# Performance work log

Hardware: AMD Instinct MI355X
Metric: run time of the kernel (lower is better)

The kernel has to match this reference:

```python
import jax, jax.numpy as jnp
import numpy as np

B, T, D, E, K = 8, 2048, 1024, 8, 2
CAP = int(B * T * K / E * 1.0)  # capacity per expert = 4096


def setup_inputs() -> dict:
    key = jax.random.key(0)
    ks = jax.random.split(key, 12)
    s = 0.02
    return {
        "x": jax.random.normal(ks[0], (B, T, D), jnp.float32),
        "noise": jax.random.normal(ks[1], (B, T, E), jnp.float32),
        "Wr": jax.random.normal(ks[2], (D, E), jnp.float32) * s,
        "br": jnp.zeros((E,), jnp.float32),
        "Wn": jax.random.normal(ks[3], (D, E), jnp.float32) * s,
        "bn": jnp.zeros((E,), jnp.float32),
        "W1": jax.random.normal(ks[4], (E, D, 4 * D), jnp.float32) * s,
        "b1": jnp.zeros((E, 4 * D), jnp.float32),
        "W2": jax.random.normal(ks[5], (E, 4 * D, D), jnp.float32) * s,
        "b2": jnp.zeros((E, D), jnp.float32),
    }


def reference(x, noise, Wr, br, Wn, bn, W1, b1, W2, b2):
    # Noisy top-k router
    logits = jnp.einsum("btd,de->bte", x, Wr) + br
    noise_logits = jnp.einsum("btd,de->bte", x, Wn) + bn
    noisy = logits + noise * jax.nn.softplus(noise_logits)
    top_v, top_i = jax.lax.top_k(noisy, K)           # [B,T,K]
    gates = jax.nn.softmax(top_v, axis=-1)           # softmax over sparse (-inf elsewhere) == softmax over top-k values

    N = B * T
    flat_x = x.reshape(N, D)
    ti = top_i.reshape(N, K)
    route = jnp.zeros((N, E), x.dtype).at[jnp.arange(N)[:, None], ti].set(gates.reshape(N, K))

    upd = jnp.zeros_like(flat_x)
    for i in range(E):
        mask = (ti == i).any(axis=-1)                 # [N] tokens routed to expert i
        rank = jnp.cumsum(mask) - 1                   # arrival-order rank (matches torch.nonzero order)
        keep = mask & (rank < CAP)                    # capacity dropping: first CAP tokens
        pos, = jnp.nonzero(keep, size=CAP, fill_value=0)
        valid = jnp.arange(CAP) < keep.sum()
        xe = flat_x[pos]                              # [CAP, D]
        h = jax.nn.relu(xe @ W1[i] + b1[i])           # [CAP, 4D]
        out = h @ W2[i] + b2[i]                       # [CAP, D]
        gate = route[pos, i] * valid                  # zero gate for padded slots
        upd = upd.at[pos].add(out * gate[:, None])
    return upd.reshape(B, T, D)
```

## Files before the change

kernel.cpp:

```cpp
#include <hip/hip_runtime.h>

#define N_TOK 16384
#define DMODEL 1024
#define NEXP 8
#define CAP 4096
#define HDIM 4096

typedef unsigned short ushort_t;
typedef unsigned int u32;
typedef __attribute__((ext_vector_type(8))) _Float16 half8;
typedef __attribute__((ext_vector_type(8))) ushort_t ushort8;
typedef __attribute__((ext_vector_type(4))) float f32x4;

__device__ inline ushort_t f2h_bits(float f) {
  _Float16 h = (_Float16)f;
  union { _Float16 h; ushort_t u; } cv;
  cv.h = h;
  return cv.u;
}
__device__ inline float h2f(ushort_t u) {
  union { ushort_t u; _Float16 h; } cv;
  cv.u = u;
  return (float)cv.h;
}

__device__ inline void gll16(void* lds, const void* g) {
  __builtin_amdgcn_global_load_lds((const __attribute__((address_space(1))) u32*)g,
                                   (__attribute__((address_space(3))) u32*)lds,
                                   16, 0, 0);
}

__global__ __launch_bounds__(256) void routerW_prep(
    const float* __restrict__ Wr, const float* __restrict__ Wn,
    float* __restrict__ wrT, float* __restrict__ wnT) {
  int i = blockIdx.x * 256 + threadIdx.x;
  int d = i >> 3, e = i & 7;
  wrT[e * DMODEL + d] = Wr[i];
  wnT[e * DMODEL + d] = Wn[i];
}

__global__ __launch_bounds__(256, 4) void router_kernel(
    const float* __restrict__ x, const float* __restrict__ noise,
    const float* __restrict__ wrT, const float* __restrict__ wnT,
    const float* __restrict__ br, const float* __restrict__ bn,
    int* __restrict__ topi, float* __restrict__ tgate) {
  int tid = threadIdx.x;
  int wave = tid >> 6, lane = tid & 63;
  int grp0 = blockIdx.x * 4 + wave;
  for (int grp = grp0; grp < N_TOK / 4; grp += gridDim.x * 4) {
    int t0 = grp * 4;
    float aR[4][NEXP], aN[4][NEXP];
#pragma unroll
    for (int tt = 0; tt < 4; ++tt)
#pragma unroll
      for (int e = 0; e < NEXP; ++e) { aR[tt][e] = 0.f; aN[tt][e] = 0.f; }
#pragma unroll 2
    for (int it = 0; it < 16; ++it) {
      int d = it * 64 + lane;
      float xv0 = x[(size_t)t0 * DMODEL + d];
      float xv1 = x[(size_t)(t0 + 1) * DMODEL + d];
      float xv2 = x[(size_t)(t0 + 2) * DMODEL + d];
      float xv3 = x[(size_t)(t0 + 3) * DMODEL + d];
#pragma unroll
      for (int e = 0; e < NEXP; ++e) {
        float wr = wrT[e * DMODEL + d];
        float wn = wnT[e * DMODEL + d];
        aR[0][e] = fmaf(xv0, wr, aR[0][e]);
        aR[1][e] = fmaf(xv1, wr, aR[1][e]);
        aR[2][e] = fmaf(xv2, wr, aR[2][e]);
        aR[3][e] = fmaf(xv3, wr, aR[3][e]);
        aN[0][e] = fmaf(xv0, wn, aN[0][e]);
        aN[1][e] = fmaf(xv1, wn, aN[1][e]);
        aN[2][e] = fmaf(xv2, wn, aN[2][e]);
        aN[3][e] = fmaf(xv3, wn, aN[3][e]);
      }
    }
#pragma unroll
    for (int tt = 0; tt < 4; ++tt)
#pragma unroll
      for (int e = 0; e < NEXP; ++e)
#pragma unroll
        for (int off = 32; off > 0; off >>= 1) {
          aR[tt][e] += __shfl_xor(aR[tt][e], off);
          aN[tt][e] += __shfl_xor(aN[tt][e], off);
        }
#pragma unroll
    for (int tt = 0; tt < 4; ++tt) {
      if (lane == tt) {
        int t = t0 + tt;
        float v0 = -1e30f, v1 = -1e30f;
        int i0 = 0, i1 = 0;
#pragma unroll
        for (int e = 0; e < NEXP; ++e) {
          float lg = aR[tt][e] + br[e];
          float nl = aN[tt][e] + bn[e];
          float sp = fmaxf(nl, 0.f) + log1pf(expf(-fabsf(nl)));
          float nz = fmaf(noise[(size_t)t * NEXP + e], sp, lg);
          if (nz > v0) { v1 = v0; i1 = i0; v0 = nz; i0 = e; }
          else if (nz > v1) { v1 = nz; i1 = e; }
        }
        float e1 = expf(v1 - v0);
        float s = 1.f + e1;
        topi[t * 2] = i0;
        topi[t * 2 + 1] = i1;
        tgate[t * 2] = 1.f / s;
        tgate[t * 2 + 1] = e1 / s;
      }
    }
  }
}

__global__ __launch_bounds__(1024) void scan_kernel(
    const int* __restrict__ topi, const float* __restrict__ tgate,
    int* __restrict__ tokL, float* __restrict__ gateL, int* __restrict__ counts,
    int* __restrict__ slotOf) {
  __shared__ int s[NEXP][1024];
  __shared__ int run[NEXP][1024];
  int t = threadIdx.x;
#pragma unroll
  for (int e = 0; e < NEXP; ++e) s[e][t] = 0;
#pragma unroll
  for (int i = 0; i < 16; ++i) {
    int n = t * 16 + i;
    s[topi[n * 2]][t]++;
    s[topi[n * 2 + 1]][t]++;
  }
  int myc[NEXP];
#pragma unroll
  for (int e = 0; e < NEXP; ++e) myc[e] = s[e][t];
  __syncthreads();
  for (int off = 1; off < 1024; off <<= 1) {
    int v[NEXP];
#pragma unroll
    for (int e = 0; e < NEXP; ++e) v[e] = (t >= off) ? s[e][t - off] : 0;
    __syncthreads();
#pragma unroll
    for (int e = 0; e < NEXP; ++e) s[e][t] += v[e];
    __syncthreads();
  }
#pragma unroll
  for (int e = 0; e < NEXP; ++e) run[e][t] = s[e][t] - myc[e];
  if (t == 1023) {
#pragma unroll
    for (int e = 0; e < NEXP; ++e) counts[e] = (s[e][1023] < CAP) ? s[e][1023] : CAP;
  }
#pragma unroll
  for (int i = 0; i < 16; ++i) {
    int n = t * 16 + i;
#pragma unroll
    for (int k = 0; k < 2; ++k) {
      int e = topi[n * 2 + k];
      int slot = run[e][t]++;
      if (slot < CAP) {
        tokL[e * CAP + slot] = n;
        gateL[e * CAP + slot] = tgate[n * 2 + k];
        slotOf[n * 2 + k] = e * CAP + slot;
      } else {
        slotOf[n * 2 + k] = -1;
      }
    }
  }
}

__global__ __launch_bounds__(256) void gather_kernel(
    const float* __restrict__ x, const int* __restrict__ tokL,
    const int* __restrict__ counts, int e0, ushort_t* __restrict__ Xg_base,
    size_t xg_es) {
  int e = e0 + blockIdx.z;
  const int* etok = tokL + e * CAP;
  ushort_t* Xg = Xg_base + (size_t)blockIdx.z * xg_es;
  int ne = counts[e];
  int slot = blockIdx.x * 2 + (threadIdx.x >> 7);
  if (slot >= ne) return;
  int tok = etok[slot];
  int c = (threadIdx.x & 127) * 8;
  const float4* src = (const float4*)(x + (size_t)tok * DMODEL + c);
  float4 v0 = src[0], v1 = src[1];
  ushort8 o;
  o[0] = f2h_bits(v0.x); o[1] = f2h_bits(v0.y); o[2] = f2h_bits(v0.z); o[3] = f2h_bits(v0.w);
  o[4] = f2h_bits(v1.x); o[5] = f2h_bits(v1.y); o[6] = f2h_bits(v1.z); o[7] = f2h_bits(v1.w);
  *(ushort8*)(Xg + (size_t)slot * DMODEL + c) = o;
}

__global__ __launch_bounds__(256) void transpose_cvt_kernel(
    const float* __restrict__ in_base, ushort_t* __restrict__ out_base,
    int R, int C) {
  __shared__ ushort_t ldsT[64 * 66];
  const float* in = in_base + (size_t)blockIdx.z * R * C;
  ushort_t* out = out_base + (size_t)blockIdx.z * R * C;
  int t = threadIdx.x;
  int c0 = blockIdx.x * 64, r0 = blockIdx.y * 64;
  int rr = t >> 4, cc = (t & 15) * 4;
#pragma unroll
  for (int p = 0; p < 4; ++p) {
    int row = r0 + p * 16 + rr;
    float4 v = *(const float4*)&in[(size_t)row * C + c0 + cc];
    ldsT[(cc + 0) * 66 + p * 16 + rr] = f2h_bits(v.x);
    ldsT[(cc + 1) * 66 + p * 16 + rr] = f2h_bits(v.y);
    ldsT[(cc + 2) * 66 + p * 16 + rr] = f2h_bits(v.z);
    ldsT[(cc + 3) * 66 + p * 16 + rr] = f2h_bits(v.w);
  }
  __syncthreads();
  int c_o = t >> 2, r_ch = (t & 3) * 16;
  ushort8 o0, o1;
#pragma unroll
  for (int m = 0; m < 8; ++m) {
    o0[m] = ldsT[c_o * 66 + r_ch + m];
    o1[m] = ldsT[c_o * 66 + r_ch + 8 + m];
  }
  ushort_t* dst = out + (size_t)(c0 + c_o) * R + r0 + r_ch;
  *(ushort8*)dst = o0;
  *(ushort8*)(dst + 8) = o1;
}

#define MFMA_Q(QM, QN, FA, FB)                                                      \
  _Pragma("unroll") for (int mp = 0; mp < 4; ++mp)                                  \
  _Pragma("unroll") for (int np = 0; np < 2; ++np)                                  \
  _Pragma("unroll") for (int ks = 0; ks < 2; ++ks)                                  \
    acc[QM][QN][mp][np] = __builtin_amdgcn_mfma_f32_16x16x32_f16(                   \
        FA[mp][ks], FB[np][ks], acc[QM][QN][mp][np], 0, 0, 0);

template <int EPI>
__global__ __launch_bounds__(512, 2) void moe_gemm256(
    const ushort_t* __restrict__ A_all, size_t a_es,
    const ushort_t* __restrict__ B_all, size_t b_es, int Kdim,
    const int* __restrict__ counts, int e0,
    const float* __restrict__ bias_base, int bias_stride,
    ushort_t* __restrict__ HY_base, size_t hy_es) {
  extern __shared__ char ldsc[];
  int flat = blockIdx.x;
  int ez = flat & 3;
  int local = flat >> 2;
  int row, col;
  if (EPI == 0) { col = local >> 4; row = local & 15; }
  else          { row = local >> 2; col = local & 3; }
  int e = e0 + ez;
  int ne = counts[e];
  int row0 = row * 256;
  if (row0 >= ne) return;
  int col0 = col * 256;

  const char* Ab = (const char*)(A_all + (size_t)ez * a_es) + (size_t)row0 * Kdim * 2;
  const char* Bb = (const char*)(B_all + (size_t)ez * b_es) + (size_t)col0 * Kdim * 2;
  const size_t gstrA = (size_t)Kdim * 2;

  int tid = threadIdx.x;
  int wave = tid >> 6, lane = tid & 63;
  int wm = wave >> 2, wn = wave & 3;
  int lr = lane & 15, lg = lane >> 4;

  f32x4 acc[2][2][4][2];
#pragma unroll
  for (int qm = 0; qm < 2; ++qm)
#pragma unroll
    for (int qn = 0; qn < 2; ++qn)
#pragma unroll
      for (int mp = 0; mp < 4; ++mp)
#pragma unroll
        for (int np = 0; np < 2; ++np) acc[qm][qn][mp][np] = f32x4{0.f, 0.f, 0.f, 0.f};

  auto STAGE = [&](char* obuf, int half, int tt) {
    const char* gb = (half < 2) ? (Ab + (size_t)(half * 128) * gstrA)
                                : (Bb + (size_t)((half - 2) * 128) * gstrA);
    gb += (size_t)tt * 128;
    char* lb = obuf + half * 16384 + wave * 1024;
#pragma unroll
    for (int i = 0; i < 2; ++i) {
      int o = (i * 512 + tid) * 16;
      int r = o >> 7;
      int lc = ((o >> 4) & 7) ^ (r & 7);
      gll16(lb + i * 8192, gb + (size_t)r * gstrA + lc * 16);
    }
  };
  auto LDA = [&](const char* buf, int qm, int mp, int ks) -> half8 {
    int r = qm * 128 + wm * 64 + mp * 16 + lr;
    int c = ((ks * 4 + lg) ^ (r & 7)) * 16;
    return *(const half8*)(buf + r * 128 + c);
  };
  auto LDB = [&](const char* buf, int qn, int np, int ks) -> half8 {
    int r = qn * 128 + wn * 32 + np * 16 + lr;
    int c = ((ks * 4 + lg) ^ (r & 7)) * 16;
    return *(const half8*)(buf + 32768 + r * 128 + c);
  };

  int NT = Kdim >> 6;
  STAGE(ldsc, 0, 0); STAGE(ldsc, 2, 0); STAGE(ldsc, 1, 0); STAGE(ldsc, 3, 0);
  asm volatile("s_waitcnt vmcnt(0)" ::: "memory");
  __builtin_amdgcn_s_barrier();

  half8 fA0[4][2], fA1[4][2], fB0[2][2], fB1[2][2];
  for (int t = 0; t < NT; ++t) {
    char* bufc = ldsc + (t & 1) * 65536;
    char* obufc = ldsc + ((t & 1) ^ 1) * 65536;
    bool pf = (t + 1 < NT);
#pragma unroll
    for (int mp = 0; mp < 4; ++mp)
#pragma unroll
      for (int ks = 0; ks < 2; ++ks) fA0[mp][ks] = LDA(bufc, 0, mp, ks);
#pragma unroll
    for (int np = 0; np < 2; ++np)
#pragma unroll
      for (int ks = 0; ks < 2; ++ks) fB0[np][ks] = LDB(bufc, 0, np, ks);
#pragma unroll
    for (int np = 0; np < 2; ++np)
#pragma unroll
      for (int ks = 0; ks < 2; ++ks) fB1[np][ks] = LDB(bufc, 1, np, ks);
#pragma unroll
    for (int mp = 0; mp < 4; ++mp)
#pragma unroll
      for (int ks = 0; ks < 2; ++ks) fA1[mp][ks] = LDA(bufc, 1, mp, ks);
    if (pf) {
      STAGE(obufc, 0, t + 1); STAGE(obufc, 2, t + 1);
      STAGE(obufc, 1, t + 1); STAGE(obufc, 3, t + 1);
    }
    __builtin_amdgcn_s_setprio(1);
    MFMA_Q(0, 0, fA0, fB0);
    MFMA_Q(0, 1, fA0, fB1);
    MFMA_Q(1, 0, fA1, fB0);
    MFMA_Q(1, 1, fA1, fB1);
    __builtin_amdgcn_s_setprio(0);
    if (pf) {
      asm volatile("s_waitcnt vmcnt(0)" ::: "memory");
      __builtin_amdgcn_s_barrier();
    }
  }

  const float* bias = bias_base + (size_t)e * bias_stride;
  int lq = lg * 4;
  if (EPI == 0) {
    ushort_t* Hp = HY_base + (size_t)ez * hy_es;
#pragma unroll
    for (int qm = 0; qm < 2; ++qm)
#pragma unroll
      for (int qn = 0; qn < 2; ++qn)
#pragma unroll
        for (int np = 0; np < 2; ++np) {
          int colx = col0 + qn * 128 + wn * 32 + np * 16 + lr;
          float bv = bias[colx];
#pragma unroll
          for (int mp = 0; mp < 4; ++mp)
#pragma unroll
            for (int j = 0; j < 4; ++j) {
              int rowx = row0 + qm * 128 + wm * 64 + mp * 16 + lq + j;
              float v = acc[qm][qn][mp][np][j] + bv;
              Hp[(size_t)rowx * HDIM + colx] = f2h_bits(fmaxf(v, 0.f));
            }
        }
  } else {
    ushort_t* Yp = HY_base + (size_t)e * hy_es;
#pragma unroll
    for (int qm = 0; qm < 2; ++qm)
#pragma unroll
      for (int qn = 0; qn < 2; ++qn)
#pragma unroll
        for (int np = 0; np < 2; ++np) {
          int colx = col0 + qn * 128 + wn * 32 + np * 16 + lr;
          float bv = bias[colx];
#pragma unroll
          for (int mp = 0; mp < 4; ++mp)
#pragma unroll
            for (int j = 0; j < 4; ++j) {
              int rowx = row0 + qm * 128 + wm * 64 + mp * 16 + lq + j;
              if (rowx < ne)
                Yp[(size_t)rowx * DMODEL + colx] = f2h_bits(acc[qm][qn][mp][np][j] + bv);
            }
        }
  }
}

template <int EPI>
__global__ __launch_bounds__(256) void moe_gemm(
    const ushort_t* __restrict__ A_base, size_t a_es,
    const ushort_t* __restrict__ B_base, size_t b_es, int Kdim,
    int nez, int ny, int nxg,
    const int* __restrict__ counts, int e0,
    const float* __restrict__ bias_base, int bias_stride,
    ushort_t* __restrict__ H_base, size_t h_es,
    ushort_t* __restrict__ Yh,
    const int* __restrict__ tokL, const float* __restrict__ gateL,
    float* __restrict__ out) {
  int flat = blockIdx.x;
  int ez = flat % nez;
  int local = flat / nez;
  int gsz = ny * nxg;
  int g = local / gsz, rem = local % gsz;
  int row = rem / nxg, xi = rem % nxg;
  int col = g * nxg + xi;
  int e = e0 + ez;
  int ne = counts[e];
  int row0 = row * 128;
  if (row0 >= ne) return;
  int col0 = col * 128;
  const ushort_t* A = A_base + (size_t)ez * a_es;
  const ushort_t* Bt = B_base + (size_t)ez * b_es;
  const float* bias = bias_base + (size_t)e * bias_stride;
  __shared__ __align__(16) ushort_t lds_a[128 * 32];
  __shared__ __align__(16) ushort_t lds_b[128 * 32];
  int tid = threadIdx.x, wave = tid >> 6, lane = tid & 63;
  int wr = wave >> 1, wc = wave & 1;
  f32x4 acc[4][4];
#pragma unroll
  for (int m = 0; m < 4; ++m)
#pragma unroll
    for (int n = 0; n < 4; ++n) acc[m][n] = f32x4{0.f, 0.f, 0.f, 0.f};
  int srow = lane >> 2;
  int soff = (lane & 3) * 16;
  const char* Ab = (const char*)A;
  const char* Bb = (const char*)Bt;
  size_t stride = (size_t)Kdim * 2;
  int lr = lane & 15, lk = (lane >> 4) * 8;
  for (int kt = 0; kt < Kdim; kt += 32) {
#pragma unroll
    for (int i = 0; i < 2; ++i) {
      int c = wave + i * 4;
      gll16((char*)lds_a + c * 1024,
            Ab + (size_t)(row0 + c * 16 + srow) * stride + (size_t)kt * 2 + soff);
      gll16((char*)lds_b + c * 1024,
            Bb + (size_t)(col0 + c * 16 + srow) * stride + (size_t)kt * 2 + soff);
    }
    __syncthreads();
    half8 af[4], bfr[4];
#pragma unroll
    for (int m = 0; m < 4; ++m)
      af[m] = *(const half8*)&lds_a[(wr * 64 + m * 16 + lr) * 32 + lk];
#pragma unroll
    for (int n = 0; n < 4; ++n)
      bfr[n] = *(const half8*)&lds_b[(wc * 64 + n * 16 + lr) * 32 + lk];
#pragma unroll
    for (int m = 0; m < 4; ++m)
#pragma unroll
      for (int n = 0; n < 4; ++n)
        acc[m][n] = __builtin_amdgcn_mfma_f32_16x16x32_f16(af[m], bfr[n], acc[m][n], 0, 0, 0);
    __syncthreads();
  }
  int lq = (lane >> 4) * 4;
  if (EPI == 0) {
    ushort_t* H = H_base + (size_t)ez * h_es;
#pragma unroll
    for (int n = 0; n < 4; ++n) {
      int col_ = col0 + wc * 64 + n * 16 + lr;
      float bv = bias[col_];
#pragma unroll
      for (int m = 0; m < 4; ++m) {
#pragma unroll
        for (int j = 0; j < 4; ++j) {
          int r = row0 + wr * 64 + m * 16 + lq + j;
          float v = acc[m][n][j] + bv;
          H[(size_t)r * HDIM + col_] = f2h_bits(fmaxf(v, 0.f));
        }
      }
    }
  } else {
    const int* etok = tokL + e * CAP;
    const float* egate = gateL + e * CAP;
    float bv[4];
#pragma unroll
    for (int n = 0; n < 4; ++n) bv[n] = bias[col0 + wc * 64 + n * 16 + lr];
#pragma unroll
    for (int m = 0; m < 4; ++m) {
#pragma unroll
      for (int j = 0; j < 4; ++j) {
        int r = row0 + wr * 64 + m * 16 + lq + j;
        if (r < ne) {
          int tok = etok[r];
          float gt = egate[r];
#pragma unroll
          for (int n = 0; n < 4; ++n) {
            int col_ = col0 + wc * 64 + n * 16 + lr;
            atomicAdd(out + (size_t)tok * DMODEL + col_, (acc[m][n][j] + bv[n]) * gt);
          }
        }
      }
    }
  }
}

__global__ __launch_bounds__(256) void combine_kernel(
    const ushort_t* __restrict__ Yh, const int* __restrict__ slotOf,
    const float* __restrict__ tgate, float* __restrict__ out) {
  int n = blockIdx.x * 2 + (threadIdx.x >> 7);
  int d = (threadIdx.x & 127) * 8;
  int s0 = slotOf[n * 2], s1 = slotOf[n * 2 + 1];
  float g0 = tgate[n * 2], g1 = tgate[n * 2 + 1];
  float acc[8];
#pragma unroll
  for (int j = 0; j < 8; ++j) acc[j] = 0.f;
  if (s0 >= 0) {
    ushort8 v = *(const ushort8*)(Yh + (size_t)s0 * DMODEL + d);
#pragma unroll
    for (int j = 0; j < 8; ++j) acc[j] = fmaf(g0, h2f(v[j]), acc[j]);
  }
  if (s1 >= 0) {
    ushort8 v = *(const ushort8*)(Yh + (size_t)s1 * DMODEL + d);
#pragma unroll
    for (int j = 0; j < 8; ++j) acc[j] = fmaf(g1, h2f(v[j]), acc[j]);
  }
  float4* o = (float4*)(out + (size_t)n * DMODEL + d);
  o[0] = float4{acc[0], acc[1], acc[2], acc[3]};
  o[1] = float4{acc[4], acc[5], acc[6], acc[7]};
}

extern "C" void kernel_launch(void* const* d_in, const int* in_sizes, int n_in,
                              void* d_out, int out_size, void* d_ws, size_t ws_size,
                              hipStream_t stream) {
  const float* x = (const float*)d_in[0];
  const float* noise = (const float*)d_in[1];
  const float* Wr = (const float*)d_in[2];
  const float* br = (const float*)d_in[3];
  const float* Wn = (const float*)d_in[4];
  const float* bn = (const float*)d_in[5];
  const float* W1 = (const float*)d_in[6];
  const float* b1 = (const float*)d_in[7];
  const float* W2 = (const float*)d_in[8];
  const float* b2 = (const float*)d_in[9];
  float* out = (float*)d_out;

  char* ws = (char*)d_ws;
  int* topi = (int*)ws;              ws += (size_t)N_TOK * 2 * 4;
  float* tgate = (float*)ws;         ws += (size_t)N_TOK * 2 * 4;
  int* tokL = (int*)ws;              ws += (size_t)NEXP * CAP * 4;
  float* gateL = (float*)ws;         ws += (size_t)NEXP * CAP * 4;
  int* slotOf = (int*)ws;            ws += (size_t)N_TOK * 2 * 4;
  int* counts = (int*)ws;            ws += 256;
  float* wrT_g = (float*)ws;         ws += (size_t)NEXP * DMODEL * 4;
  float* wnT_g = (float*)ws;         ws += (size_t)NEXP * DMODEL * 4;

  const size_t XG_E = (size_t)CAP * DMODEL;
  const size_t W1_E = (size_t)HDIM * DMODEL;
  const size_t W2_E = (size_t)DMODEL * HDIM;
  const size_t H_E  = (size_t)CAP * HDIM;
  const size_t Y_E  = (size_t)CAP * DMODEL;

  routerW_prep<<<32, 256, 0, stream>>>(Wr, Wn, wrT_g, wnT_g);
  router_kernel<<<1024, 256, 0, stream>>>(x, noise, wrT_g, wnT_g, br, bn, topi, tgate);
  scan_kernel<<<1, 1024, 0, stream>>>(topi, tgate, tokL, gateL, counts, slotOf);

  size_t used = (size_t)(ws - (char*)d_ws);
  size_t need_fast = 2ull * NEXP * (XG_E + W1_E + W2_E + Y_E) + 2ull * 4 * H_E + 1024;
  bool fast = (ws_size - used) >= need_fast;

  if (fast) {
    ushort_t* Xg_all = (ushort_t*)ws;   ws += 2ull * NEXP * XG_E;
    ushort_t* W1t_all = (ushort_t*)ws;  ws += 2ull * NEXP * W1_E;
    ushort_t* W2t_all = (ushort_t*)ws;  ws += 2ull * NEXP * W2_E;
    ushort_t* H4 = (ushort_t*)ws;       ws += 2ull * 4 * H_E;
    ushort_t* Yh = (ushort_t*)ws;       ws += 2ull * NEXP * Y_E;

    hipFuncSetAttribute(reinterpret_cast<const void*>(moe_gemm256<0>),
                        hipFuncAttributeMaxDynamicSharedMemorySize, 131072);
    hipFuncSetAttribute(reinterpret_cast<const void*>(moe_gemm256<1>),
                        hipFuncAttributeMaxDynamicSharedMemorySize, 131072);

    gather_kernel<<<dim3(CAP / 2, 1, NEXP), 256, 0, stream>>>(
        x, tokL, counts, 0, Xg_all, XG_E);
    transpose_cvt_kernel<<<dim3(HDIM / 64, DMODEL / 64, NEXP), 256, 0, stream>>>(
        W1, W1t_all, DMODEL, HDIM);
    transpose_cvt_kernel<<<dim3(DMODEL / 64, HDIM / 64, NEXP), 256, 0, stream>>>(
        W2, W2t_all, HDIM, DMODEL);
    for (int g = 0; g < 2; ++g) {
      int e0 = g * 4;
      moe_gemm256<0><<<dim3(4 * 16 * 16), 512, 131072, stream>>>(
          Xg_all + (size_t)e0 * XG_E, XG_E, W1t_all + (size_t)e0 * W1_E, W1_E,
          DMODEL, counts, e0, b1, HDIM, H4, H_E);
      moe_gemm256<1><<<dim3(4 * 16 * 4), 512, 131072, stream>>>(
          H4, H_E, W2t_all + (size_t)e0 * W2_E, W2_E,
          HDIM, counts, e0, b2, DMODEL, Yh, Y_E);
    }
    combine_kernel<<<dim3(N_TOK / 2), 256, 0, stream>>>(Yh, slotOf, tgate, out);
  } else {
    hipMemsetAsync(d_out, 0, (size_t)out_size * sizeof(float), stream);
    ushort_t* Xg = (ushort_t*)ws;   ws += 2ull * XG_E;
    ushort_t* W1t = (ushort_t*)ws;  ws += 2ull * W1_E;
    ushort_t* W2t = (ushort_t*)ws;  ws += 2ull * W2_E;
    ushort_t* H = (ushort_t*)ws;    ws += 2ull * H_E;
    for (int e = 0; e < NEXP; ++e) {
      gather_kernel<<<dim3(CAP / 2, 1, 1), 256, 0, stream>>>(
          x, tokL, counts, e, Xg, 0);
      transpose_cvt_kernel<<<dim3(HDIM / 64, DMODEL / 64, 1), 256, 0, stream>>>(
          W1 + (size_t)e * W1_E, W1t, DMODEL, HDIM);
      transpose_cvt_kernel<<<dim3(DMODEL / 64, HDIM / 64, 1), 256, 0, stream>>>(
          W2 + (size_t)e * W2_E, W2t, HDIM, DMODEL);
      moe_gemm<0><<<dim3(32 * 32), 256, 0, stream>>>(
          Xg, 0, W1t, 0, DMODEL, 1, 32, 1, counts, e, b1, HDIM,
          H, 0, nullptr, nullptr, nullptr, nullptr);
      moe_gemm<1><<<dim3(32 * 8), 256, 0, stream>>>(
          H, 0, W2t, 0, HDIM, 1, 32, 4, counts, e, b2, DMODEL,
          nullptr, 0, nullptr, tokL, gateL, out);
    }
  }
}
```

Before: 872.4 us.

## Deepen GEMM main loop to a two-tile-ahead, quadrant-interleaved prefetch schedule

After: 877.5 us. Within noise of the previous version (+0.6%).

```diff
diff --git a/kernel.cpp b/kernel.cpp
--- a/kernel.cpp
+++ b/kernel.cpp
@@ -284,15 +284,22 @@
   };
 
   int NT = Kdim >> 6;
-  STAGE(ldsc, 0, 0); STAGE(ldsc, 2, 0); STAGE(ldsc, 1, 0); STAGE(ldsc, 3, 0);
-  asm volatile("s_waitcnt vmcnt(0)" ::: "memory");
+  STAGE(ldsc, 0, 0); STAGE(ldsc, 2, 0); STAGE(ldsc, 3, 0); STAGE(ldsc, 1, 0);
+  if (NT > 1) {
+    char* b1p = ldsc + 65536;
+    STAGE(b1p, 0, 1); STAGE(b1p, 2, 1); STAGE(b1p, 3, 1);
+    asm volatile("s_waitcnt vmcnt(6)" ::: "memory");
+  } else {
+    asm volatile("s_waitcnt vmcnt(0)" ::: "memory");
+  }
   __builtin_amdgcn_s_barrier();
 
   half8 fA0[4][2], fA1[4][2], fB0[2][2], fB1[2][2];
   for (int t = 0; t < NT; ++t) {
-    char* bufc = ldsc + (t & 1) * 65536;
-    char* obufc = ldsc + ((t & 1) ^ 1) * 65536;
-    bool pf = (t + 1 < NT);
+    const char* bufc = ldsc + (t & 1) * 65536;
+    char* nbuf = ldsc + ((t + 1) & 1) * 65536;
+    char* nnbuf = ldsc + (t & 1) * 65536;
+    bool p1 = (t + 1 < NT), p2 = (t + 2 < NT);
 #pragma unroll
     for (int mp = 0; mp < 4; ++mp)
 #pragma unroll
@@ -301,28 +308,46 @@
     for (int np = 0; np < 2; ++np)
 #pragma unroll
       for (int ks = 0; ks < 2; ++ks) fB0[np][ks] = LDB(bufc, 0, np, ks);
-#pragma unroll
-    for (int np = 0; np < 2; ++np)
-#pragma unroll
-      for (int ks = 0; ks < 2; ++ks) fB1[np][ks] = LDB(bufc, 1, np, ks);
-#pragma unroll
-    for (int mp = 0; mp < 4; ++mp)
-#pragma unroll
-      for (int ks = 0; ks < 2; ++ks) fA1[mp][ks] = LDA(bufc, 1, mp, ks);
-    if (pf) {
-      STAGE(obufc, 0, t + 1); STAGE(obufc, 2, t + 1);
-      STAGE(obufc, 1, t + 1); STAGE(obufc, 3, t + 1);
-    }
+    if (p1) STAGE(nbuf, 1, t + 1);
+    __builtin_amdgcn_s_barrier();
+    asm volatile("s_waitcnt lgkmcnt(0)" ::: "memory");
     __builtin_amdgcn_s_setprio(1);
     MFMA_Q(0, 0, fA0, fB0);
+    __builtin_amdgcn_s_setprio(0);
+    __builtin_amdgcn_s_barrier();
+#pragma unroll
+    for (int np = 0; np < 2; ++np)
+#pragma unroll
+      for (int ks = 0; ks < 2; ++ks) fB1[np][ks] = LDB(bufc, 1, np, ks);
+    if (p2) STAGE(nnbuf, 0, t + 2);
+    __builtin_amdgcn_s_barrier();
+    asm volatile("s_waitcnt lgkmcnt(0)" ::: "memory");
+    __builtin_amdgcn_s_setprio(1);
     MFMA_Q(0, 1, fA0, fB1);
+    __builtin_amdgcn_s_setprio(0);
+    __builtin_amdgcn_s_barrier();
+#pragma unroll
+    for (int mp = 0; mp < 4; ++mp)
+#pragma unroll
+      for (int ks = 0; ks < 2; ++ks) fA1[mp][ks] = LDA(bufc, 1, mp, ks);
+    if (p2) STAGE(nnbuf, 2, t + 2);
+    __builtin_amdgcn_s_barrier();
+    asm volatile("s_waitcnt lgkmcnt(0)" ::: "memory");
+    __builtin_amdgcn_s_setprio(1);
     MFMA_Q(1, 0, fA1, fB0);
+    __builtin_amdgcn_s_setprio(0);
+    __builtin_amdgcn_s_barrier();
+    if (p2) {
+      STAGE(nnbuf, 3, t + 2);
+      asm volatile("s_waitcnt vmcnt(6)" ::: "memory");
+    } else {
+      asm volatile("s_waitcnt vmcnt(0)" ::: "memory");
+    }
+    __builtin_amdgcn_s_barrier();
+    __builtin_amdgcn_s_setprio(1);
     MFMA_Q(1, 1, fA1, fB1);
     __builtin_amdgcn_s_setprio(0);
-    if (pf) {
-      asm volatile("s_waitcnt vmcnt(0)" ::: "memory");
-      __builtin_amdgcn_s_barrier();
-    }
+    __builtin_amdgcn_s_barrier();
   }
 
   const float* bias = bias_base + (size_t)e * bias_stride;
```
